# Optimization experiments

Hardware: AMD Instinct MI355X
Metric: run time of the kernel (lower is better)

The kernel has to match this reference:

```python
import jax, jax.numpy as jnp
import numpy as np

TAU = 10.0          # tau_init
R_MAX = 8           # max(groupconvs)
GROUPCONVS = (4, 8)
PADS = (0, 8)       # (k - spat_red)//2 for k in (17, 33), spat_red = 33 - 2*8 = 17
NEG_SLOPE = 0.01    # LeakyReLU default


def lrelu(t):
    return jnp.where(t >= 0, t, NEG_SLOPE * t)


def rotate_kernel(w, theta):
    """Rotate square kernels w:[N,k,k] by theta, matching torch
    F.affine_grid + F.grid_sample (bilinear, zero padding, align_corners=False)."""
    N, k, _ = w.shape
    coords = (2.0 * jnp.arange(k) + 1.0) / k - 1.0  # normalized pixel centers
    gy, gx = jnp.meshgrid(coords, coords, indexing='ij')
    c, s = jnp.cos(theta), jnp.sin(theta)
    sx = c * gx - s * gy
    sy = s * gx + c * gy
    fx = ((sx + 1.0) * k - 1.0) / 2.0
    fy = ((sy + 1.0) * k - 1.0) / 2.0
    x0 = jnp.floor(fx).astype(jnp.int32)
    y0 = jnp.floor(fy).astype(jnp.int32)
    wf = w.reshape(N, k * k)

    def gather(yi, xi):
        valid = ((yi >= 0) & (yi < k) & (xi >= 0) & (xi < k)).astype(w.dtype)
        idx = jnp.clip(yi, 0, k - 1) * k + jnp.clip(xi, 0, k - 1)
        return wf[:, idx.reshape(-1)].reshape(N, k, k) * valid

    wx1 = fx - x0
    wy1 = fy - y0
    return (gather(y0, x0) * (1 - wy1) * (1 - wx1)
            + gather(y0, x0 + 1) * (1 - wy1) * wx1
            + gather(y0 + 1, x0) * wy1 * (1 - wx1)
            + gather(y0 + 1, x0 + 1) * wy1 * wx1)


def group_conv(x, w, b, pad):
    """GroupConv with input_rot_dim=1: x [B,1,H,W], w [O,1,1,k,k] -> [B,O,R_MAX,H',W']."""
    O, k = w.shape[0], w.shape[-1]
    w2 = w.reshape(O, k, k)
    angles = (2.0 * jnp.pi / R_MAX) * jnp.arange(R_MAX)
    tw = jax.vmap(lambda th: rotate_kernel(w2, th))(angles)   # [R,O,k,k]
    tw = jnp.transpose(tw, (1, 0, 2, 3)).reshape(O * R_MAX, 1, k, k)
    y = jax.lax.conv_general_dilated(x, tw, (1, 1), [(pad, pad), (pad, pad)],
                                     dimension_numbers=('NCHW', 'OIHW', 'NCHW'))
    B, _, H, W = y.shape
    return y.reshape(B, O, R_MAX, H, W) + b[None, :, None, None, None]


def conv1x1(h, w, b):
    # 1x1x1 Conv3d: h [B,C,R,H,W], w [O,C], b [O]
    return jnp.einsum('bcrhw,oc->borhw', h, w) + b[None, :, None, None, None]


def scatter_sum(outs, weights, axis):
    """slice_scatter-based alignment: embed smaller-rdim tensors into the
    largest one at stride max_dim//dim, weight, and sum."""
    max_out = outs[-1]
    md = max_out.shape[axis]
    total = max_out * weights[-1]
    for i, o in enumerate(outs[:-1]):
        step = md // o.shape[axis]
        idx = tuple(slice(None, None, step) if a == axis else slice(None)
                    for a in range(max_out.ndim))
        total = total + jnp.zeros_like(max_out).at[idx].set(o) * weights[i]
    return total


OFFSETS = np.array([0, np.pi / 4, np.pi / 2, 3 * np.pi / 4, np.pi,
                    -3 * np.pi / 4, -np.pi / 2, -np.pi / 4], dtype=np.float32)


def _forward(x, ksize_weight, rdim_weight, conv1_w0, conv1_b0, conv1_w1, conv1_b1,
             conv2_w, conv2_b, conva_w, conva_b, convz_w, convz_b,
             g_ksize, g_rdim, g_attn):
    # gumbel-softmax over kernel sizes (soft, tau=TAU)
    alphas = jax.nn.softmax((ksize_weight + g_ksize) / TAU)
    x_out = (alphas[0] * lrelu(group_conv(x, conv1_w0, conv1_b0, PADS[0]))
             + alphas[1] * lrelu(group_conv(x, conv1_w1, conv1_b1, PADS[1])))
    xs_out = [x_out[:, :, ::R_MAX // r] for r in GROUPCONVS]
    hs = [lrelu(conv1x1(xo, conv2_w[i], conv2_b[i])) for i, xo in enumerate(xs_out)]
    attns = [conv1x1(h, conva_w[i], conva_b[i])[:, 0] for i, h in enumerate(hs)]
    betas = jax.nn.softmax((rdim_weight + g_rdim) / TAU)
    attn = scatter_sum(attns, betas, axis=1)          # [B,R,H,W]
    offsets = jnp.asarray(OFFSETS)
    sigma = np.pi  # theta_prior; Normal(0, sigma) log-prob at offsets
    p_r = (-0.5 * (offsets / sigma) ** 2 - np.float32(np.log(sigma))
           - np.float32(0.5 * np.log(2.0 * np.pi)))[:, None, None]
    attn = attn + p_r
    B = attn.shape[0]
    flat = attn.reshape(B, -1)
    q_t_r = jax.nn.log_softmax(flat, axis=1).reshape(attn.shape)
    # F.gumbel_softmax(a, dim=-1) with default tau=1
    a_sampled = jax.nn.softmax(flat + g_attn, axis=-1).reshape(attn.shape)
    zs = [conv1x1(h, convz_w[i], convz_b[i]) for i, h in enumerate(hs)]
    z = scatter_sum(zs, betas, axis=2)                # [B,2L,R,H,W]
    # faithful to source: `thetas = [c_r(h) for c_r, h in zip(self.conv_z, hs)]`
    # reuses conv_z, so pre-refinement theta == z
    theta_pre = z
    rotation_offset = jnp.broadcast_to(offsets[None, :, None, None], a_sampled.shape)
    theta = jnp.stack((theta_pre[:, 0] + rotation_offset, theta_pre[:, 1]), axis=1)
    return attn, q_t_r, p_r, a_sampled, offsets, theta, z


def setup_inputs() -> dict:
    key = jax.random.key(0)
    ks = jax.random.split(key, 16)
    B, n, KN, L = 8, 64, 128, 2
    gum = lambda k, shape: -jnp.log(-jnp.log(
        jax.random.uniform(k, shape, jnp.float32, 1e-10, 1.0)))
    return {
        'x': jax.random.normal(ks[0], (B, 1, n, n), jnp.float32),
        'ksize_weight': 0.001 * jax.random.normal(ks[1], (2,), jnp.float32),
        'rdim_weight': 0.001 * jax.random.normal(ks[2], (2,), jnp.float32),
        'conv1_w0': 0.02 * jax.random.normal(ks[3], (KN, 1, 1, 17, 17), jnp.float32),
        'conv1_b0': 0.01 * jax.random.normal(ks[4], (KN,), jnp.float32),
        'conv1_w1': 0.02 * jax.random.normal(ks[5], (KN, 1, 1, 33, 33), jnp.float32),
        'conv1_b1': 0.01 * jax.random.normal(ks[6], (KN,), jnp.float32),
        'conv2_w': (1.0 / np.sqrt(KN)) * jax.random.normal(ks[7], (2, KN, KN), jnp.float32),
        'conv2_b': 0.01 * jax.random.normal(ks[8], (2, KN), jnp.float32),
        'conva_w': (1.0 / np.sqrt(KN)) * jax.random.normal(ks[9], (2, 1, KN), jnp.float32),
        'conva_b': 0.01 * jax.random.normal(ks[10], (2, 1), jnp.float32),
        'convz_w': (1.0 / np.sqrt(KN)) * jax.random.normal(ks[11], (2, 2 * L, KN), jnp.float32),
        'convz_b': 0.01 * jax.random.normal(ks[12], (2, 2 * L), jnp.float32),
        'g_ksize': gum(ks[13], (2,)),
        'g_rdim': gum(ks[14], (2,)),
        'g_attn': gum(ks[15], (B, R_MAX * 48 * 48)),
    }


def reference(x, ksize_weight, rdim_weight, conv1_w0, conv1_b0, conv1_w1, conv1_b1,
              conv2_w, conv2_b, conva_w, conva_b, convz_w, convz_b,
              g_ksize, g_rdim, g_attn):
    return _forward(x, ksize_weight, rdim_weight, conv1_w0, conv1_b0, conv1_w1,
                    conv1_b1, conv2_w, conv2_b, conva_w, conva_b, convz_w, convz_b,
                    g_ksize, g_rdim, g_attn)
```

## Files before the change

kernel.cpp:

```cpp
#include <hip/hip_runtime.h>
#include <hip/hip_bf16.h>
#include <math.h>

#define PI_D 3.14159265358979323846

typedef __attribute__((ext_vector_type(8))) short bf16x8;
typedef __attribute__((ext_vector_type(4))) float f32x4;
typedef __attribute__((ext_vector_type(4))) unsigned int u32x4;

#define OFF_SCAL   0u
#define OFF_W0T    4u
#define OFF_W1T    36996u
#define OFF_W2B    176388u
#define OFF_BF     192772u
#define OFF_XOUTB  1093892u
#define OFF_A0     10531076u
#define OFF_A1     10604804u
#define OFF_Z0     10752260u
#define OFF_Z1     11047172u

#define NS33 42
#define NS17 13

__device__ __forceinline__ float off_r(int r) {
  int m = (r <= 4) ? r : r - 8;
  return (float)(PI_D / 4.0) * (float)m;
}
__device__ __forceinline__ float lrelu_f(float v) { return (v >= 0.f) ? v : 0.01f * v; }
__device__ __forceinline__ short f2bf(float f) {
  __bf16 h = (__bf16)f;
  return __builtin_bit_cast(short, h);
}

__global__ void k_prep1(const float* __restrict__ kw, const float* __restrict__ gk,
                        const float* __restrict__ rw, const float* __restrict__ gr,
                        const float* __restrict__ w0, const float* __restrict__ w1,
                        const float* __restrict__ w2, float* __restrict__ scal,
                        float* __restrict__ w0T, float* __restrict__ w1T,
                        short* __restrict__ w2b) {
  int idx = blockIdx.x * blockDim.x + threadIdx.x;
  if (idx == 0) {
    float a0 = (kw[0] + gk[0]) * 0.1f, a1 = (kw[1] + gk[1]) * 0.1f;
    float m = fmaxf(a0, a1);
    float e0 = expf(a0 - m), e1 = expf(a1 - m), inv = 1.f / (e0 + e1);
    scal[0] = e0 * inv; scal[1] = e1 * inv;
    float b0 = (rw[0] + gr[0]) * 0.1f, b1 = (rw[1] + gr[1]) * 0.1f;
    m = fmaxf(b0, b1);
    e0 = expf(b0 - m); e1 = expf(b1 - m); inv = 1.f / (e0 + e1);
    scal[2] = e0 * inv; scal[3] = e1 * inv;
  }
  if (idx < 289 * 128) {
    int o = idx & 127, pos = idx >> 7;
    w0T[pos * 128 + o] = w0[o * 289 + pos];
    return;
  }
  idx -= 289 * 128;
  if (idx < 1089 * 128) {
    int o = idx & 127, pos = idx >> 7;
    w1T[pos * 128 + o] = w1[o * 1089 + pos];
    return;
  }
  idx -= 1089 * 128;
  if (idx < 2 * 128 * 128) w2b[idx] = f2bf(w2[idx]);
}

__global__ void k_prep2(const float* __restrict__ w0T, const float* __restrict__ w1T,
                        short* __restrict__ bfrag) {
  int t = blockIdx.x * blockDim.x + threadIdx.x;
  int o = t & 127;
  int q = t >> 7;
  int kb = q & 3; q >>= 2;
  int c = q % 55; int r = q / 55;
  float theta = (float)(PI_D / 4.0) * (float)r;
  float cth = cosf(theta), sth = sinf(theta);
  short out[8];
#pragma unroll
  for (int j = 0; j < 8; ++j) {
    float val = 0.f;
    int kk, k, dy, dx;
    const float* wT;
    if (c < NS33) { kk = 32 * c + 8 * kb + j; k = 33; dy = kk / 40; dx = kk - 40 * dy; wT = w1T; }
    else          { kk = 32 * (c - NS33) + 8 * kb + j; k = 17; dy = kk / 24; dx = kk - 24 * dy; wT = w0T; }
    if (dy < k && dx < k) {
      float cy = (2.0f * (float)dy + 1.0f) / (float)k - 1.0f;
      float cx = (2.0f * (float)dx + 1.0f) / (float)k - 1.0f;
      float sx = cth * cx - sth * cy;
      float sy = sth * cx + cth * cy;
      float fx = ((sx + 1.0f) * (float)k - 1.0f) * 0.5f;
      float fy = ((sy + 1.0f) * (float)k - 1.0f) * 0.5f;
      float x0f = floorf(fx), y0f = floorf(fy);
      int x0 = (int)x0f, y0 = (int)y0f;
      float wx1 = fx - x0f, wy1 = fy - y0f;
      float acc = 0.f;
#define CORNER(Y, X, CW) { int yy = (Y), xx = (X); \
      if (yy >= 0 && yy < k && xx >= 0 && xx < k) acc += wT[(yy * k + xx) * 128 + o] * (CW); }
      CORNER(y0,     x0,     (1.f - wy1) * (1.f - wx1));
      CORNER(y0,     x0 + 1, (1.f - wy1) * wx1);
      CORNER(y0 + 1, x0,     wy1 * (1.f - wx1));
      CORNER(y0 + 1, x0 + 1, wy1 * wx1);
#undef CORNER
      val = acc;
    }
    out[j] = f2bf(val);
  }
  *(bf16x8*)(bfrag + (size_t)t * 8) =
      (bf16x8){out[0], out[1], out[2], out[3], out[4], out[5], out[6], out[7]};
}

#define TDW 3080
#define SHW 1544
__global__ __launch_bounds__(256, 4) void k_conv_mfma(
    const float* __restrict__ x, const short* __restrict__ bfrag,
    const float* __restrict__ b17, const float* __restrict__ b33,
    const float* __restrict__ scal, short* __restrict__ xoutb) {
  __shared__ __align__(16) unsigned int lds[4352];
  unsigned short* lA = (unsigned short*)lds;
  unsigned short* lB = (unsigned short*)(lds + SHW);
  int blk = blockIdx.x;
  int pt = blk % 36; int t2 = blk / 36; int r = t2 & 7, b = t2 >> 3;
  int p0 = pt * 64;
  int ybase = p0 / 48;
  int tid = threadIdx.x;
  for (int idx = tid; idx < TDW; idx += 256) {
    int ty = idx / 88, tx = idx - ty * 88;
    int gy = ybase + ty - 8, gx = tx - 8;
    float v = 0.f;
    if (gy >= 0 && gy < 64 && gx >= 0 && gx < 64) v = x[(b * 64 + gy) * 64 + gx];
    unsigned short h = (unsigned short)f2bf(v);
    lA[idx] = h;
    if (idx > 0) lB[idx - 1] = h;
  }
  if (tid == 0) lB[TDW - 1] = 0;
  __syncthreads();

  int lane = tid & 63, w = tid >> 6;
  int wm = w >> 1, wn = w & 1;
  int kc = lane >> 4;
  int ln = lane & 15;
  int mloc[2];
#pragma unroll
  for (int mf = 0; mf < 2; ++mf) {
    int p = p0 + wm * 32 + mf + 2 * ln;
    int ym = p / 48, xm = p - ym * 48;
    mloc[mf] = (ym - ybase) * 88 + xm;
  }
  const short* bb = bfrag + (size_t)r * (55 * 4 * 128 * 8);
  int nb0 = wn * 64;

  f32x4 acc33[2][4];
#pragma unroll
  for (int mf = 0; mf < 2; ++mf)
#pragma unroll
    for (int nf = 0; nf < 4; ++nf) acc33[mf][nf] = (f32x4){0.f, 0.f, 0.f, 0.f};

#define LOADB(dst, cg)                                                          \
  {                                                                             \
    _Pragma("unroll")                                                           \
    for (int nf = 0; nf < 4; ++nf)                                              \
      dst[nf] = *(const bf16x8*)(bb + ((size_t)((cg)*4 + kc) * 128 + nb0 + nf * 16 + ln) * 8); \
  }
#define READA(dst, mf, vv)                                                      \
  {                                                                             \
    int bd_ = ((vv) >> 1) + ((mf) ? SHW : 0);                                   \
    u32x4 uv_ = {lds[bd_], lds[bd_ + 1], lds[bd_ + 2], lds[bd_ + 3]};           \
    dst = __builtin_bit_cast(bf16x8, uv_);                                      \
  }

  {
    int dxb = 8 * kc;
    int off = dxb;
    bf16x8 bc[4], bn[4];
    LOADB(bc, 0);
    for (int c = 0; c < NS33; ++c) {
      if (c + 1 < NS33) LOADB(bn, c + 1);
      bf16x8 a0, a1;
      READA(a0, 0, mloc[0] + off);
      READA(a1, 1, mloc[1] + off);
#pragma unroll
      for (int nf = 0; nf < 4; ++nf) {
        acc33[0][nf] = __builtin_amdgcn_mfma_f32_16x16x32_bf16(a0, bc[nf], acc33[0][nf], 0, 0, 0);
        acc33[1][nf] = __builtin_amdgcn_mfma_f32_16x16x32_bf16(a1, bc[nf], acc33[1][nf], 0, 0, 0);
      }
#pragma unroll
      for (int nf = 0; nf < 4; ++nf) bc[nf] = bn[nf];
      int nd = dxb + 32;
      int wr = (nd >= 40);
      dxb = wr ? nd - 40 : nd;
      off += wr ? 80 : 32;
    }
  }

  f32x4 acc17[2][4];
#pragma unroll
  for (int mf = 0; mf < 2; ++mf)
#pragma unroll
    for (int nf = 0; nf < 4; ++nf) acc17[mf][nf] = (f32x4){0.f, 0.f, 0.f, 0.f};
  {
    int t8 = 8 * kc;
    int dy0 = t8 / 24;
    int dxb = t8 - 24 * dy0;
    int off = (8 + dy0) * 88 + 8 + dxb;
    for (int c = 0; c < NS17; ++c) {
      bf16x8 bc[4];
      LOADB(bc, NS33 + c);
      bf16x8 a0, a1;
      READA(a0, 0, mloc[0] + off);
      READA(a1, 1, mloc[1] + off);
#pragma unroll
      for (int nf = 0; nf < 4; ++nf) {
        acc17[0][nf] = __builtin_amdgcn_mfma_f32_16x16x32_bf16(a0, bc[nf], acc17[0][nf], 0, 0, 0);
        acc17[1][nf] = __builtin_amdgcn_mfma_f32_16x16x32_bf16(a1, bc[nf], acc17[1][nf], 0, 0, 0);
      }
      int nd = dxb + 8;
      int wr = (nd >= 24);
      dxb = wr ? nd - 24 : nd;
      off += wr ? 160 : 96;
    }
  }
#undef LOADB
#undef READA

  __syncthreads();
  unsigned short* sOut = (unsigned short*)lds;
  float a0s = scal[0], a1s = scal[1];
#pragma unroll
  for (int nf = 0; nf < 4; ++nf) {
    int n = nb0 + nf * 16 + ln;
    float bb17 = b17[n], bb33 = b33[n];
    int sw = n ^ (kc << 4);
#pragma unroll
    for (int mf = 0; mf < 2; ++mf) {
#pragma unroll
      for (int i = 0; i < 4; ++i) {
        int px = wm * 32 + mf + 8 * kc + 2 * i;
        float v = a0s * lrelu_f(acc17[mf][nf][i] + bb17)
                + a1s * lrelu_f(acc33[mf][nf][i] + bb33);
        sOut[px * 136 + sw] = (unsigned short)f2bf(v);
      }
    }
  }
  __syncthreads();
  size_t gbase = ((size_t)(b * 8 + r) * 2304 + p0) * 128;
#pragma unroll
  for (int pass = 0; pass < 4; ++pass) {
    int L16 = pass * 256 + tid;
    int px = L16 >> 4, u = L16 & 15;
    int kc3 = (px >> 3) & 3;
    int pu = u ^ (kc3 << 1);
    const unsigned int* lp = lds + px * 68 + pu * 4;
    u32x4 vv = {lp[0], lp[1], lp[2], lp[3]};
    *(u32x4*)(xoutb + gbase + (size_t)L16 * 8) = vv;
  }
}

__global__ __launch_bounds__(256, 4) void k_pw_mfma(
    const short* __restrict__ xoutb, const short* __restrict__ w2b_,
    const float* __restrict__ b2_, const float* __restrict__ wa_,
    const float* __restrict__ ba_, const float* __restrict__ wz_,
    const float* __restrict__ bz_,
    float* __restrict__ a0buf, float* __restrict__ z0buf,
    float* __restrict__ a1buf, float* __restrict__ z1buf) {
  __shared__ float sA[64];
  __shared__ float sZ[4][64];
  int blk = blockIdx.x;
  int i1 = (blk >= 1152);
  int lblk = i1 ? blk - 1152 : blk;
  int nR = i1 ? 8 : 4, rstep = i1 ? 1 : 2;
  const short* w2b = w2b_ + (i1 ? 128 * 128 : 0);
  const float* b2 = b2_ + (i1 ? 128 : 0);
  const float* wa = wa_ + (i1 ? 128 : 0);
  const float* ba = ba_ + i1;
  const float* wz = wz_ + (i1 ? 512 : 0);
  const float* bz = bz_ + (i1 ? 4 : 0);
  float* attn_out = i1 ? a1buf : a0buf;
  float* z_out = i1 ? z1buf : z0buf;

  int pblk = lblk % 36;
  int t = lblk / 36;
  int rl = t % nR;
  int b = t / nR;
  int pix0 = pblk * 64;
  int tid = threadIdx.x;
  int lane = tid & 63, w = tid >> 6;
  int kc = lane >> 4, ln = lane & 15;
  int pwave = pix0 + w * 16;
  const short* arow = xoutb + ((size_t)(b * 8 + rl * rstep) * 2304 + pwave) * 128;

  f32x4 acc[8];
#pragma unroll
  for (int nf = 0; nf < 8; ++nf) acc[nf] = (f32x4){0.f, 0.f, 0.f, 0.f};
#pragma unroll
  for (int s = 0; s < 4; ++s) {
    bf16x8 a = *(const bf16x8*)(arow + ln * 128 + s * 32 + kc * 8);
#pragma unroll
    for (int nf = 0; nf < 8; ++nf) {
      bf16x8 bv = *(const bf16x8*)(w2b + (nf * 16 + ln) * 128 + s * 32 + kc * 8);
      acc[nf] = __builtin_amdgcn_mfma_f32_16x16x32_bf16(a, bv, acc[nf], 0, 0, 0);
    }
  }

  float attn_acc[4] = {0.f, 0.f, 0.f, 0.f};
  float zacc[4][4];
#pragma unroll
  for (int j = 0; j < 4; ++j)
#pragma unroll
    for (int q = 0; q < 4; ++q) zacc[j][q] = 0.f;
#pragma unroll
  for (int nf = 0; nf < 8; ++nf) {
    int n = nf * 16 + ln;
    float bb2 = b2[n];
    float wan = wa[n];
    float wz0 = wz[n], wz1 = wz[128 + n], wz2 = wz[256 + n], wz3 = wz[384 + n];
#pragma unroll
    for (int q = 0; q < 4; ++q) {
      float h = lrelu_f(acc[nf][q] + bb2);
      attn_acc[q] = fmaf(wan, h, attn_acc[q]);
      zacc[0][q] = fmaf(wz0, h, zacc[0][q]);
      zacc[1][q] = fmaf(wz1, h, zacc[1][q]);
      zacc[2][q] = fmaf(wz2, h, zacc[2][q]);
      zacc[3][q] = fmaf(wz3, h, zacc[3][q]);
    }
  }
#pragma unroll
  for (int off = 1; off < 16; off <<= 1) {
#pragma unroll
    for (int q = 0; q < 4; ++q) {
      attn_acc[q] += __shfl_xor(attn_acc[q], off);
#pragma unroll
      for (int j = 0; j < 4; ++j) zacc[j][q] += __shfl_xor(zacc[j][q], off);
    }
  }
  if (ln == 0) {
    float ba0 = ba[0];
#pragma unroll
    for (int q = 0; q < 4; ++q) {
      int px = w * 16 + kc * 4 + q;
      sA[px] = attn_acc[q] + ba0;
#pragma unroll
      for (int j = 0; j < 4; ++j) sZ[j][px] = zacc[j][q] + bz[j];
    }
  }
  __syncthreads();
  int px = tid & 63, jj = tid >> 6;
  if (jj == 0)
    attn_out[((size_t)b * nR + rl) * 2304 + pix0 + px] = sA[px];
  z_out[(((size_t)b * 4 + jj) * nR + rl) * 2304 + pix0 + px] = sZ[jj][px];
}

__global__ void k_attn_combine(const float* __restrict__ a0buf, const float* __restrict__ a1buf,
                               const float* __restrict__ scal, float* __restrict__ out0,
                               float* __restrict__ out2, float* __restrict__ out4) {
  int idx = blockIdx.x * blockDim.x + threadIdx.x;
  if (idx < 8) {
    float off = off_r(idx);
    out4[idx] = off;
    float q = off / (float)PI_D;
    out2[idx] = -0.5f * q * q - logf((float)PI_D) - 0.5f * logf(2.0f * (float)PI_D);
  }
  if (idx >= 147456) return;
  int pix = idx % 2304;
  int t = idx / 2304;
  int r = t & 7, b = t >> 3;
  float v = scal[3] * a1buf[idx];
  if (!(r & 1)) v += scal[2] * a0buf[((size_t)b * 4 + (r >> 1)) * 2304 + pix];
  float q = off_r(r) / (float)PI_D;
  v += -0.5f * q * q - logf((float)PI_D) - 0.5f * logf(2.0f * (float)PI_D);
  out0[idx] = v;
}

__global__ __launch_bounds__(1024) void k_softmax(const float* __restrict__ out0,
                                                  const float* __restrict__ g,
                                                  float* __restrict__ out1,
                                                  float* __restrict__ out3) {
  int b = blockIdx.x;
  int tid = threadIdx.x;
  const float* v = out0 + (size_t)b * 18432;
  const float* gb = g + (size_t)b * 18432;
  float vl[18], gl[18];
  float m1 = -1e30f, m2 = -1e30f;
#pragma unroll
  for (int t = 0; t < 18; ++t) {
    float vv = v[tid + (t << 10)];
    float gg = gb[tid + (t << 10)];
    vl[t] = vv;
    gl[t] = vv + gg;
    m1 = fmaxf(m1, vv);
    m2 = fmaxf(m2, gl[t]);
  }
  __shared__ float red[32];
  for (int off = 32; off > 0; off >>= 1) {
    m1 = fmaxf(m1, __shfl_xor(m1, off));
    m2 = fmaxf(m2, __shfl_xor(m2, off));
  }
  int wid = tid >> 6, lane = tid & 63;
  if (lane == 0) { red[wid] = m1; red[wid + 16] = m2; }
  __syncthreads();
  float M1 = red[0], M2 = red[16];
#pragma unroll
  for (int w = 1; w < 16; ++w) { M1 = fmaxf(M1, red[w]); M2 = fmaxf(M2, red[w + 16]); }
  __syncthreads();
  float s1 = 0.f, s2 = 0.f;
#pragma unroll
  for (int t = 0; t < 18; ++t) { s1 += expf(vl[t] - M1); s2 += expf(gl[t] - M2); }
  for (int off = 32; off > 0; off >>= 1) {
    s1 += __shfl_xor(s1, off);
    s2 += __shfl_xor(s2, off);
  }
  if (lane == 0) { red[wid] = s1; red[wid + 16] = s2; }
  __syncthreads();
  float S1 = 0.f, S2 = 0.f;
#pragma unroll
  for (int w = 0; w < 16; ++w) { S1 += red[w]; S2 += red[w + 16]; }
  float lse = M1 + logf(S1);
  float inv2 = 1.0f / S2;
  float* o1 = out1 + (size_t)b * 18432;
  float* o3 = out3 + (size_t)b * 18432;
#pragma unroll
  for (int t = 0; t < 18; ++t) {
    o1[tid + (t << 10)] = vl[t] - lse;
    o3[tid + (t << 10)] = expf(gl[t] - M2) * inv2;
  }
}

__global__ void k_ztheta(const float* __restrict__ z0buf, const float* __restrict__ z1buf,
                         const float* __restrict__ scal, float* __restrict__ out5,
                         float* __restrict__ out6) {
  int idx = blockIdx.x * blockDim.x + threadIdx.x;
  if (idx >= 589824) return;
  int pix = idx % 2304;
  int t = idx / 2304;
  int r = t & 7;
  t >>= 3;
  int c = t & 3;
  int b = t >> 2;
  float v = scal[3] * z1buf[idx];
  if (!(r & 1)) v += scal[2] * z0buf[(((size_t)b * 4 + c) * 4 + (r >> 1)) * 2304 + pix];
  out6[idx] = v;
  if (c == 0)      out5[(((size_t)b * 2 + 0) * 8 + r) * 2304 + pix] = v + off_r(r);
  else if (c == 1) out5[(((size_t)b * 2 + 1) * 8 + r) * 2304 + pix] = v;
}

extern "C" void kernel_launch(void* const* d_in, const int* in_sizes, int n_in,
                              void* d_out, int out_size, void* d_ws, size_t ws_size,
                              hipStream_t stream) {
  const float* x   = (const float*)d_in[0];
  const float* ksz = (const float*)d_in[1];
  const float* rdw = (const float*)d_in[2];
  const float* w0  = (const float*)d_in[3];
  const float* b0  = (const float*)d_in[4];
  const float* w1  = (const float*)d_in[5];
  const float* b1  = (const float*)d_in[6];
  const float* w2  = (const float*)d_in[7];
  const float* b2  = (const float*)d_in[8];
  const float* wa  = (const float*)d_in[9];
  const float* ba  = (const float*)d_in[10];
  const float* wz  = (const float*)d_in[11];
  const float* bz  = (const float*)d_in[12];
  const float* gks = (const float*)d_in[13];
  const float* grd = (const float*)d_in[14];
  const float* gat = (const float*)d_in[15];
  float* out = (float*)d_out;
  float* ws  = (float*)d_ws;

  float* scal = ws + OFF_SCAL;
  float* w0T  = ws + OFF_W0T;
  float* w1T  = ws + OFF_W1T;
  short* w2b  = (short*)(ws + OFF_W2B);
  short* bfr  = (short*)(ws + OFF_BF);
  short* xoutb = (short*)(ws + OFF_XOUTB);
  float* a0b  = ws + OFF_A0;
  float* a1b  = ws + OFF_A1;
  float* z0b  = ws + OFF_Z0;
  float* z1b  = ws + OFF_Z1;

  float* out0 = out;
  float* out1 = out + 147456;
  float* out2 = out + 294912;
  float* out3 = out + 294920;
  float* out4 = out + 442376;
  float* out5 = out + 442384;
  float* out6 = out + 737296;

  k_prep1<<<817, 256, 0, stream>>>(ksz, gks, rdw, grd, w0, w1, w2, scal, w0T, w1T, w2b);
  k_prep2<<<880, 256, 0, stream>>>(w0T, w1T, bfr);
  k_conv_mfma<<<2304, 256, 0, stream>>>(x, bfr, b0, b1, scal, xoutb);
  k_pw_mfma<<<3456, 256, 0, stream>>>(xoutb, w2b, b2, wa, ba, wz, bz,
                                      a0b, z0b, a1b, z1b);
  k_attn_combine<<<576, 256, 0, stream>>>(a0b, a1b, scal, out0, out2, out4);
  k_softmax<<<8, 1024, 0, stream>>>(out0, gat, out1, out3);
  k_ztheta<<<2304, 256, 0, stream>>>(z0b, z1b, scal, out5, out6);
}
```

Measured before the change: 267.5 us.

## Double conv M-tile per block and reorder K units by row/chunk

The conv MFMA kernel now covers 128 output pixels per block instead of 64, so each wave issues four A fragments per K step against the same B fragments. This halves B-fragment global loads per output and halves the grid. The K dimension is also remapped into (row, 8-wide chunk) units ordered even rows then odd rows, with prep2 changed to match. This removes the padded 40/24-wide row layout and the per-step offset arithmetic. The cost is doubled accumulator registers and LDS, which lowers launch bounds occupancy to 2 blocks per CU.

```diff
diff --git a/kernel.cpp b/kernel.cpp
--- a/kernel.cpp
+++ b/kernel.cpp
@@ -30,6 +30,17 @@
 __device__ __forceinline__ short f2bf(float f) {
   __bf16 h = (__bf16)f;
   return __builtin_bit_cast(short, h);
+}
+
+__device__ __forceinline__ void unit33(int u, int& dy, int& ch) {
+  if (u < 85)       { dy = (u % 17) * 2;            ch = u / 17; }
+  else if (u < 165) { int v = u - 85; dy = (v & 15) * 2 + 1; ch = v >> 4; }
+  else              { dy = 33; ch = 0; }
+}
+__device__ __forceinline__ void unit17(int u, int& dy, int& ch) {
+  if (u < 27)      { dy = (u % 9) * 2;             ch = u / 9; }
+  else if (u < 51) { int v = u - 27; dy = (v & 7) * 2 + 1; ch = v >> 3; }
+  else             { dy = 17; ch = 0; }
 }
 
 __global__ void k_prep1(const float* __restrict__ kw, const float* __restrict__ gk,
@@ -77,10 +88,11 @@
 #pragma unroll
   for (int j = 0; j < 8; ++j) {
     float val = 0.f;
-    int kk, k, dy, dx;
+    int k, dy, ch;
     const float* wT;
-    if (c < NS33) { kk = 32 * c + 8 * kb + j; k = 33; dy = kk / 40; dx = kk - 40 * dy; wT = w1T; }
-    else          { kk = 32 * (c - NS33) + 8 * kb + j; k = 17; dy = kk / 24; dx = kk - 24 * dy; wT = w0T; }
+    if (c < NS33) { unit33(4 * c + kb, dy, ch); k = 33; wT = w1T; }
+    else          { unit17(4 * (c - NS33) + kb, dy, ch); k = 17; wT = w0T; }
+    int dx = 8 * ch + j;
     if (dy < k && dx < k) {
       float cy = (2.0f * (float)dy + 1.0f) / (float)k - 1.0f;
       float cx = (2.0f * (float)dx + 1.0f) / (float)k - 1.0f;
@@ -107,18 +119,20 @@
       (bf16x8){out[0], out[1], out[2], out[3], out[4], out[5], out[6], out[7]};
 }
 
-#define TDW 3080
-#define SHW 1544
-__global__ __launch_bounds__(256, 4) void k_conv_mfma(
+#define TDW 3256
+#define LBOFF 1628
+__global__ __launch_bounds__(256, 2) void k_conv_mfma(
     const float* __restrict__ x, const short* __restrict__ bfrag,
     const float* __restrict__ b17, const float* __restrict__ b33,
     const float* __restrict__ scal, short* __restrict__ xoutb) {
-  __shared__ __align__(16) unsigned int lds[4352];
+  __shared__ __align__(16) unsigned int lds[8704];
   unsigned short* lA = (unsigned short*)lds;
-  unsigned short* lB = (unsigned short*)(lds + SHW);
+  unsigned short* lB = (unsigned short*)(lds + LBOFF);
   int blk = blockIdx.x;
-  int pt = blk % 36; int t2 = blk / 36; int r = t2 & 7, b = t2 >> 3;
-  int p0 = pt * 64;
+  int r = blk & 7;
+  int q = blk >> 3;
+  int pt = q % 18, b = q / 18;
+  int p0 = pt * 128;
   int ybase = p0 / 48;
   int tid = threadIdx.x;
   for (int idx = tid; idx < TDW; idx += 256) {
@@ -137,19 +151,19 @@
   int wm = w >> 1, wn = w & 1;
   int kc = lane >> 4;
   int ln = lane & 15;
-  int mloc[2];
-#pragma unroll
-  for (int mf = 0; mf < 2; ++mf) {
-    int p = p0 + wm * 32 + mf + 2 * ln;
+  int mloc[4];
+#pragma unroll
+  for (int mf = 0; mf < 4; ++mf) {
+    int p = p0 + wm * 64 + (mf >> 1) * 32 + (mf & 1) + 2 * ln;
     int ym = p / 48, xm = p - ym * 48;
     mloc[mf] = (ym - ybase) * 88 + xm;
   }
   const short* bb = bfrag + (size_t)r * (55 * 4 * 128 * 8);
   int nb0 = wn * 64;
 
-  f32x4 acc33[2][4];
-#pragma unroll
-  for (int mf = 0; mf < 2; ++mf)
+  f32x4 acc33[4][4];
+#pragma unroll
+  for (int mf = 0; mf < 4; ++mf)
 #pragma unroll
     for (int nf = 0; nf < 4; ++nf) acc33[mf][nf] = (f32x4){0.f, 0.f, 0.f, 0.f};
 
@@ -159,62 +173,58 @@
     for (int nf = 0; nf < 4; ++nf)                                              \
       dst[nf] = *(const bf16x8*)(bb + ((size_t)((cg)*4 + kc) * 128 + nb0 + nf * 16 + ln) * 8); \
   }
-#define READA(dst, mf, vv)                                                      \
+#define READA(dst, par, vv)                                                     \
   {                                                                             \
-    int bd_ = ((vv) >> 1) + ((mf) ? SHW : 0);                                   \
+    int bd_ = ((vv) >> 1) + ((par) ? LBOFF : 0);                                \
     u32x4 uv_ = {lds[bd_], lds[bd_ + 1], lds[bd_ + 2], lds[bd_ + 3]};           \
     dst = __builtin_bit_cast(bf16x8, uv_);                                      \
   }
 
   {
-    int dxb = 8 * kc;
-    int off = dxb;
     bf16x8 bc[4], bn[4];
     LOADB(bc, 0);
     for (int c = 0; c < NS33; ++c) {
       if (c + 1 < NS33) LOADB(bn, c + 1);
-      bf16x8 a0, a1;
-      READA(a0, 0, mloc[0] + off);
-      READA(a1, 1, mloc[1] + off);
+      int dy, ch;
+      unit33(4 * c + kc, dy, ch);
+      int off = dy * 88 + ch * 8;
+      bf16x8 a[4];
+      READA(a[0], 0, mloc[0] + off);
+      READA(a[1], 1, mloc[1] + off);
+      READA(a[2], 0, mloc[2] + off);
+      READA(a[3], 1, mloc[3] + off);
 #pragma unroll
       for (int nf = 0; nf < 4; ++nf) {
-        acc33[0][nf] = __builtin_amdgcn_mfma_f32_16x16x32_bf16(a0, bc[nf], acc33[0][nf], 0, 0, 0);
-        acc33[1][nf] = __builtin_amdgcn_mfma_f32_16x16x32_bf16(a1, bc[nf], acc33[1][nf], 0, 0, 0);
+#pragma unroll
+        for (int mf = 0; mf < 4; ++mf)
+          acc33[mf][nf] = __builtin_amdgcn_mfma_f32_16x16x32_bf16(a[mf], bc[nf], acc33[mf][nf], 0, 0, 0);
       }
 #pragma unroll
       for (int nf = 0; nf < 4; ++nf) bc[nf] = bn[nf];
-      int nd = dxb + 32;
-      int wr = (nd >= 40);
-      dxb = wr ? nd - 40 : nd;
-      off += wr ? 80 : 32;
-    }
-  }
-
-  f32x4 acc17[2][4];
-#pragma unroll
-  for (int mf = 0; mf < 2; ++mf)
+    }
+  }
+
+  f32x4 acc17[4][4];
+#pragma unroll
+  for (int mf = 0; mf < 4; ++mf)
 #pragma unroll
     for (int nf = 0; nf < 4; ++nf) acc17[mf][nf] = (f32x4){0.f, 0.f, 0.f, 0.f};
-  {
-    int t8 = 8 * kc;
-    int dy0 = t8 / 24;
-    int dxb = t8 - 24 * dy0;
-    int off = (8 + dy0) * 88 + 8 + dxb;
-    for (int c = 0; c < NS17; ++c) {
-      bf16x8 bc[4];
-      LOADB(bc, NS33 + c);
-      bf16x8 a0, a1;
-      READA(a0, 0, mloc[0] + off);
-      READA(a1, 1, mloc[1] + off);
-#pragma unroll
-      for (int nf = 0; nf < 4; ++nf) {
-        acc17[0][nf] = __builtin_amdgcn_mfma_f32_16x16x32_bf16(a0, bc[nf], acc17[0][nf], 0, 0, 0);
-        acc17[1][nf] = __builtin_amdgcn_mfma_f32_16x16x32_bf16(a1, bc[nf], acc17[1][nf], 0, 0, 0);
-      }
-      int nd = dxb + 8;
-      int wr = (nd >= 24);
-      dxb = wr ? nd - 24 : nd;
-      off += wr ? 160 : 96;
+  for (int c = 0; c < NS17; ++c) {
+    bf16x8 bc[4];
+    LOADB(bc, NS33 + c);
+    int dy, ch;
+    unit17(4 * c + kc, dy, ch);
+    int off = (8 + dy) * 88 + 8 + ch * 8;
+    bf16x8 a[4];
+    READA(a[0], 0, mloc[0] + off);
+    READA(a[1], 1, mloc[1] + off);
+    READA(a[2], 0, mloc[2] + off);
+    READA(a[3], 1, mloc[3] + off);
+#pragma unroll
+    for (int nf = 0; nf < 4; ++nf) {
+#pragma unroll
+      for (int mf = 0; mf < 4; ++mf)
+        acc17[mf][nf] = __builtin_amdgcn_mfma_f32_16x16x32_bf16(a[mf], bc[nf], acc17[mf][nf], 0, 0, 0);
     }
   }
 #undef LOADB
@@ -229,10 +239,10 @@
     float bb17 = b17[n], bb33 = b33[n];
     int sw = n ^ (kc << 4);
 #pragma unroll
-    for (int mf = 0; mf < 2; ++mf) {
+    for (int mf = 0; mf < 4; ++mf) {
 #pragma unroll
       for (int i = 0; i < 4; ++i) {
-        int px = wm * 32 + mf + 8 * kc + 2 * i;
+        int px = wm * 64 + (mf >> 1) * 32 + (mf & 1) + 8 * kc + 2 * i;
         float v = a0s * lrelu_f(acc17[mf][nf][i] + bb17)
                 + a1s * lrelu_f(acc33[mf][nf][i] + bb33);
         sOut[px * 136 + sw] = (unsigned short)f2bf(v);
@@ -242,7 +252,7 @@
   __syncthreads();
   size_t gbase = ((size_t)(b * 8 + r) * 2304 + p0) * 128;
 #pragma unroll
-  for (int pass = 0; pass < 4; ++pass) {
+  for (int pass = 0; pass < 8; ++pass) {
     int L16 = pass * 256 + tid;
     int px = L16 >> 4, u = L16 & 15;
     int kc3 = (px >> 3) & 3;
@@ -483,7 +493,7 @@
 
   k_prep1<<<817, 256, 0, stream>>>(ksz, gks, rdw, grd, w0, w1, w2, scal, w0T, w1T, w2b);
   k_prep2<<<880, 256, 0, stream>>>(w0T, w1T, bfr);
-  k_conv_mfma<<<2304, 256, 0, stream>>>(x, bfr, b0, b1, scal, xoutb);
+  k_conv_mfma<<<1152, 256, 0, stream>>>(x, bfr, b0, b1, scal, xoutb);
   k_pw_mfma<<<3456, 256, 0, stream>>>(xoutb, w2b, b2, wa, ba, wz, bz,
                                       a0b, z0b, a1b, z1b);
   k_attn_combine<<<576, 256, 0, stream>>>(a0b, a1b, scal, out0, out2, out4);
```

After: 256.8 us. 4.0% less time.
